# Performance work log

Hardware: AMD Instinct MI355X
Metric: run time of the kernel (lower is better)

Reference implementation:

```python
import jax, jax.numpy as jnp
import numpy as np

N = 50000          # nodes
E = 800000         # edges (before self-loops)
IN_CH = 128
H1, C1 = 8, 32     # layer-1 heads / channels-per-head (concat -> 256)
H2, C2 = 1, 64     # layer-2 (out_channels=64, heads=1)
NEG_SLOPE = 0.2    # PyG GATConv default LeakyReLU slope for attention


def setup_inputs() -> dict:
    key = jax.random.key(0)
    ks = jax.random.split(key, 10)
    x = jax.random.normal(ks[0], (N, IN_CH), dtype=jnp.float32)
    edge_index = jax.random.randint(ks[1], (2, E), 0, N, dtype=jnp.int64)
    s = 0.05
    W1 = jax.random.normal(ks[2], (IN_CH, H1 * C1), dtype=jnp.float32) * s
    a_src1 = jax.random.normal(ks[3], (H1, C1), dtype=jnp.float32) * s
    a_dst1 = jax.random.normal(ks[4], (H1, C1), dtype=jnp.float32) * s
    b1 = jnp.zeros((H1 * C1,), dtype=jnp.float32)
    W2 = jax.random.normal(ks[5], (H1 * C1, H2 * C2), dtype=jnp.float32) * s
    a_src2 = jax.random.normal(ks[6], (H2, C2), dtype=jnp.float32) * s
    a_dst2 = jax.random.normal(ks[7], (H2, C2), dtype=jnp.float32) * s
    b2 = jnp.zeros((H2 * C2,), dtype=jnp.float32)
    return {"x": x, "edge_index": edge_index,
            "W1": W1, "a_src1": a_src1, "a_dst1": a_dst1, "b1": b1,
            "W2": W2, "a_src2": a_src2, "a_dst2": a_dst2, "b2": b2}


def gat_conv(x, src, dst, W, a_src, a_dst, b, heads, ch):
    """PyG GATConv (eval mode): gather -> LeakyReLU attn -> scatter-softmax -> scatter-add."""
    n = x.shape[0]
    h = (x @ W).reshape(n, heads, ch)                     # [N, H, C]
    alpha_s = jnp.einsum('nhc,hc->nh', h, a_src)          # [N, H]
    alpha_d = jnp.einsum('nhc,hc->nh', h, a_dst)
    e = jax.nn.leaky_relu(alpha_s[src] + alpha_d[dst], NEG_SLOPE)  # [E, H]
    # numerically-stable softmax over edges grouped by destination node
    emax = jax.ops.segment_max(e, dst, num_segments=n)
    e = jnp.exp(e - emax[dst])
    denom = jax.ops.segment_sum(e, dst, num_segments=n)
    alpha = e / denom[dst]                                # [E, H]
    out = jax.ops.segment_sum(h[src] * alpha[:, :, None], dst, num_segments=n)  # [N, H, C]
    return out.reshape(n, heads * ch) + b


def reference(x, edge_index, W1, a_src1, a_dst1, b1, W2, a_src2, a_dst2, b2):
    # PyG GATConv adds self-loops by default
    loops = jnp.arange(N, dtype=edge_index.dtype)
    src = jnp.concatenate([edge_index[0], loops])
    dst = jnp.concatenate([edge_index[1], loops])
    h = jax.nn.relu(gat_conv(x, src, dst, W1, a_src1, a_dst1, b1, H1, C1))
    out = jax.nn.relu(gat_conv(h, src, dst, W2, a_src2, a_dst2, b2, H2, C2))
    return out
```

## Files before the change

kernel.cpp:

```cpp
#include <hip/hip_runtime.h>
#include <math.h>

#define NEG_SLOPE 0.2f
__device__ __forceinline__ float leaky(float x) { return fmaxf(x, NEG_SLOPE * x); }

typedef _Float16 f16;
typedef _Float16 f16x2 __attribute__((ext_vector_type(2)));
typedef _Float16 f16x4 __attribute__((ext_vector_type(4)));
typedef _Float16 f16x8 __attribute__((ext_vector_type(8)));
typedef float f32x4 __attribute__((ext_vector_type(4)));

__device__ __forceinline__ int kmap(int lh, int e) {
  return (e < 4) ? lh * 4 + e : 16 + lh * 4 + (e - 4);
}

__global__ void k_count(const int* __restrict__ dst, int* __restrict__ deg, int E) {
  int e = blockIdx.x * blockDim.x + threadIdx.x;
  if (e < E) atomicAdd(&deg[dst[e]], 1);
}

#define W1_TOT (17 * 4 * 64 * 8)
#define W2_TOT (5 * 8 * 64 * 8)
__global__ __launch_bounds__(256) void k_partial_packw(const int* __restrict__ deg,
    int* __restrict__ part, int n, int nb,
    const float* __restrict__ W1, const float* __restrict__ as1f,
    const float* __restrict__ ad1f, const float* __restrict__ W2,
    const float* __restrict__ as2f, const float* __restrict__ ad2f,
    f16* __restrict__ Wp1, f16* __restrict__ Wp2) {
  if ((int)blockIdx.x < nb) {
    __shared__ int s[256];
    int i = blockIdx.x * 256 + threadIdx.x;
    s[threadIdx.x] = (i < n) ? deg[i] : 0;
    __syncthreads();
    for (int off = 128; off > 0; off >>= 1) {
      if (threadIdx.x < off) s[threadIdx.x] += s[threadIdx.x + off];
      __syncthreads();
    }
    if (threadIdx.x == 0) part[blockIdx.x] = s[0];
  }
  int tid = blockIdx.x * 256 + threadIdx.x;
  if (tid < W1_TOT) {
    int e = tid & 7, l = (tid >> 3) & 63, ks = (tid >> 9) & 3, nt = tid >> 11;
    int lh = l >> 4, li = l & 15;
    int k = ks * 32 + kmap(lh, e);
    float v;
    if (nt < 16) {
      v = W1[k * 256 + nt * 16 + li];
    } else {
      int h = li & 7;
      const float* a = (li < 8) ? (as1f + h * 32) : (ad1f + h * 32);
      v = 0.f;
      for (int j = 0; j < 32; ++j) v += W1[k * 256 + h * 32 + j] * a[j];
    }
    Wp1[tid] = (f16)v;
  } else if (tid < W1_TOT + W2_TOT) {
    int t2 = tid - W1_TOT;
    int e = t2 & 7, l = (t2 >> 3) & 63, ks = (t2 >> 9) & 7, nt = t2 >> 12;
    int lh = l >> 4, li = l & 15;
    int k = ks * 32 + kmap(lh, e);
    float v = 0.f;
    if (nt < 4) {
      v = W2[k * 64 + nt * 16 + li];
    } else if (li == 0) {
      for (int j = 0; j < 64; ++j) v += W2[k * 64 + j] * as2f[j];
    } else if (li == 1) {
      for (int j = 0; j < 64; ++j) v += W2[k * 64 + j] * ad2f[j];
    }
    Wp2[t2] = (f16)v;
  }
}

__global__ __launch_bounds__(256) void k_offs(int* __restrict__ deg,
                                              const int* __restrict__ part,
                                              int* __restrict__ offs, int n, int nb) {
  __shared__ int ps[256];
  __shared__ int s[256];
  int t = threadIdx.x;
  ps[t] = (t < nb) ? part[t] : 0;
  __syncthreads();
  for (int off = 1; off < 256; off <<= 1) {
    int u = (t >= off) ? ps[t - off] : 0;
    __syncthreads();
    ps[t] += u;
    __syncthreads();
  }
  int base = (blockIdx.x > 0) ? ps[blockIdx.x - 1] : 0;

  int i = blockIdx.x * 256 + t;
  int v = (i < n) ? deg[i] : 0;
  s[t] = v;
  __syncthreads();
  for (int off = 1; off < 256; off <<= 1) {
    int u = (t >= off) ? s[t - off] : 0;
    __syncthreads();
    s[t] += u;
    __syncthreads();
  }
  int excl = base + s[t] - v;
  if (i < n) {
    offs[i] = excl;
    deg[i] = 0;
  }
  if (i == n - 1) offs[n] = excl + v;
}

__global__ __launch_bounds__(256) void k_fill_gemm1(
    const int* __restrict__ src, const int* __restrict__ dst,
    const int* __restrict__ offs, int* __restrict__ cursor,
    int* __restrict__ col, int E, int fillBlocks,
    const float* __restrict__ x, const f16* __restrict__ Wp1,
    f16* __restrict__ h16, float* __restrict__ as, float* __restrict__ ad,
    int n, int nSlots) {
  if ((int)blockIdx.x < fillBlocks) {
    int e = blockIdx.x * 256 + threadIdx.x;
    if (e >= E) return;
    int d = dst[e];
    int pos = atomicAdd(&cursor[d], 1);
    col[offs[d] + pos] = src[e];
    return;
  }
  int slot = (blockIdx.x - fillBlocks) * 4 + (threadIdx.x >> 6);
  if (slot >= nSlots) return;
  int half = slot & 1;
  int wid = slot >> 1;
  int lane = threadIdx.x & 63, lh = lane >> 4, li = lane & 15;
  size_t arow = (size_t)min(wid * 16 + li, n - 1);
  f16x8 a[4];
#pragma unroll
  for (int ks = 0; ks < 4; ++ks) {
    float4 lo = *(const float4*)&x[arow * 128 + ks * 32 + lh * 4];
    float4 hi = *(const float4*)&x[arow * 128 + ks * 32 + 16 + lh * 4];
    a[ks][0] = (f16)lo.x; a[ks][1] = (f16)lo.y; a[ks][2] = (f16)lo.z; a[ks][3] = (f16)lo.w;
    a[ks][4] = (f16)hi.x; a[ks][5] = (f16)hi.y; a[ks][6] = (f16)hi.z; a[ks][7] = (f16)hi.w;
  }
  int rbase = wid * 16 + lh * 4;
  int ntBeg = half ? 8 : 0;
  int ntEnd = half ? 17 : 8;
  for (int nt = ntBeg; nt < ntEnd; ++nt) {
    f32x4 acc = {0.f, 0.f, 0.f, 0.f};
#pragma unroll
    for (int ks = 0; ks < 4; ++ks) {
      f16x8 b = *(const f16x8*)&Wp1[((nt * 4 + ks) * 64 + lane) * 8];
      acc = __builtin_amdgcn_mfma_f32_16x16x32_f16(a[ks], b, acc, 0, 0, 0);
    }
    if (nt < 16) {
#pragma unroll
      for (int r = 0; r < 4; ++r) {
        int rr = rbase + r;
        if (rr < n) h16[(size_t)rr * 256 + nt * 16 + li] = (f16)acc[r];
      }
    } else {
#pragma unroll
      for (int r = 0; r < 4; ++r) {
        int rr = rbase + r;
        if (rr < n) {
          if (li < 8) as[(size_t)rr * 8 + li] = acc[r];
          else        ad[(size_t)rr * 8 + (li - 8)] = acc[r];
        }
      }
    }
  }
}

__global__ __launch_bounds__(256) void k_gemm2(const f16* __restrict__ R16,
    const f16* __restrict__ Wp2, f16* __restrict__ h2,
    float* __restrict__ as, float* __restrict__ ad, int n, int nWaves) {
  int wid = blockIdx.x * 4 + (threadIdx.x >> 6);
  if (wid >= nWaves) return;
  int lane = threadIdx.x & 63, lh = lane >> 4, li = lane & 15;
  size_t arow = (size_t)min(wid * 16 + li, n - 1);
  f16x8 a[8];
#pragma unroll
  for (int ks = 0; ks < 8; ++ks) {
    f16x4 lo = *(const f16x4*)&R16[arow * 256 + ks * 32 + lh * 4];
    f16x4 hi = *(const f16x4*)&R16[arow * 256 + ks * 32 + 16 + lh * 4];
    a[ks][0] = lo[0]; a[ks][1] = lo[1]; a[ks][2] = lo[2]; a[ks][3] = lo[3];
    a[ks][4] = hi[0]; a[ks][5] = hi[1]; a[ks][6] = hi[2]; a[ks][7] = hi[3];
  }
  int rbase = wid * 16 + lh * 4;
#pragma unroll
  for (int nt = 0; nt < 5; ++nt) {
    f32x4 acc = {0.f, 0.f, 0.f, 0.f};
#pragma unroll
    for (int ks = 0; ks < 8; ++ks) {
      f16x8 b = *(const f16x8*)&Wp2[((nt * 8 + ks) * 64 + lane) * 8];
      acc = __builtin_amdgcn_mfma_f32_16x16x32_f16(a[ks], b, acc, 0, 0, 0);
    }
    if (nt < 4) {
#pragma unroll
      for (int r = 0; r < 4; ++r) {
        int rr = rbase + r;
        if (rr < n) h2[(size_t)rr * 64 + nt * 16 + li] = (f16)acc[r];
      }
    } else {
#pragma unroll
      for (int r = 0; r < 4; ++r) {
        int rr = rbase + r;
        if (rr < n) {
          if (li == 0) as[rr] = acc[r];
          else if (li == 1) ad[rr] = acc[r];
        }
      }
    }
  }
}

__global__ __launch_bounds__(256) void k_agg1(const f16* __restrict__ h16,
    const float* __restrict__ as, const float* __restrict__ ad,
    const int* __restrict__ offs, const int* __restrict__ col,
    const float* __restrict__ b, f16* __restrict__ out, int n) {
  int node = blockIdx.x * 4 + (threadIdx.x >> 6);
  if (node >= n) return;
  node = __builtin_amdgcn_readfirstlane(node);
  int lane = threadIdx.x & 63;
  int head = lane >> 3;
  int c0 = lane * 4;
  int beg = offs[node], end = offs[node + 1];
  float adn = ad[node * 8 + head];

  float denom, ax, ay, az, aw;
  {
    float w = __expf(leaky(as[node * 8 + head] + adn));
    f16x4 g = *(const f16x4*)&h16[(size_t)node * 256 + c0];
    denom = w;
    ax = w * (float)g[0]; ay = w * (float)g[1];
    az = w * (float)g[2]; aw = w * (float)g[3];
  }
  int p = beg;
  for (; p + 8 <= end; p += 8) {
    int s[8];
#pragma unroll
    for (int j = 0; j < 8; ++j) s[j] = col[p + j];
    float e[8];
#pragma unroll
    for (int j = 0; j < 8; ++j) e[j] = as[s[j] * 8 + head];
    f16x4 g[8];
#pragma unroll
    for (int j = 0; j < 8; ++j) g[j] = *(const f16x4*)&h16[(size_t)s[j] * 256 + c0];
    float w[8];
#pragma unroll
    for (int j = 0; j < 8; ++j) w[j] = __expf(leaky(e[j] + adn));
#pragma unroll
    for (int j = 0; j < 8; ++j) {
      denom += w[j];
      ax += w[j] * (float)g[j][0]; ay += w[j] * (float)g[j][1];
      az += w[j] * (float)g[j][2]; aw += w[j] * (float)g[j][3];
    }
  }
  for (; p < end; ++p) {
    int s = col[p];
    float w = __expf(leaky(as[s * 8 + head] + adn));
    f16x4 g = *(const f16x4*)&h16[(size_t)s * 256 + c0];
    denom += w;
    ax += w * (float)g[0]; ay += w * (float)g[1];
    az += w * (float)g[2]; aw += w * (float)g[3];
  }
  float inv = 1.f / denom;
  float4 bv = *(const float4*)&b[c0];
  f16x4 o;
  o[0] = (f16)fmaxf(fmaf(ax, inv, bv.x), 0.f);
  o[1] = (f16)fmaxf(fmaf(ay, inv, bv.y), 0.f);
  o[2] = (f16)fmaxf(fmaf(az, inv, bv.z), 0.f);
  o[3] = (f16)fmaxf(fmaf(aw, inv, bv.w), 0.f);
  __builtin_nontemporal_store(o, (f16x4*)&out[(size_t)node * 256 + c0]);
}

__global__ __launch_bounds__(256) void k_agg2(const f16* __restrict__ h2,
    const float* __restrict__ as, const float* __restrict__ ad,
    const int* __restrict__ offs, const int* __restrict__ col,
    const float* __restrict__ b, float* __restrict__ out, int n) {
  int node = blockIdx.x * 4 + (threadIdx.x >> 6);
  if (node >= n) return;
  node = __builtin_amdgcn_readfirstlane(node);
  int lane = threadIdx.x & 63;
  int es = lane >> 4;
  int c = lane & 15;
  int beg = offs[node], end = offs[node + 1];
  int deg = end - beg;
  float adn = ad[node];

  float a0 = 0.f, a1 = 0.f, a2 = 0.f, a3 = 0.f, wsum = 0.f;
  if (es == 0) {
    float w = __expf(leaky(as[node] + adn));
    f16x4 g = *(const f16x4*)&h2[(size_t)node * 64 + c * 4];
    wsum = w;
    a0 = w * (float)g[0]; a1 = w * (float)g[1];
    a2 = w * (float)g[2]; a3 = w * (float)g[3];
  }
  for (int base = 0; base < deg; base += 16) {
    int s[4]; float e[4]; f16x4 g[4]; float w[4];
#pragma unroll
    for (int q = 0; q < 4; ++q) {
      int idx = base + q * 4 + es;
      s[q] = (idx < deg) ? col[beg + idx] : node;
    }
#pragma unroll
    for (int q = 0; q < 4; ++q) e[q] = as[s[q]];
#pragma unroll
    for (int q = 0; q < 4; ++q) g[q] = *(const f16x4*)&h2[(size_t)s[q] * 64 + c * 4];
#pragma unroll
    for (int q = 0; q < 4; ++q) {
      int idx = base + q * 4 + es;
      w[q] = (idx < deg) ? __expf(leaky(e[q] + adn)) : 0.f;
    }
#pragma unroll
    for (int q = 0; q < 4; ++q) {
      wsum += w[q];
      a0 += w[q] * (float)g[q][0]; a1 += w[q] * (float)g[q][1];
      a2 += w[q] * (float)g[q][2]; a3 += w[q] * (float)g[q][3];
    }
  }
  a0 += __shfl_xor(a0, 16, 64); a1 += __shfl_xor(a1, 16, 64);
  a2 += __shfl_xor(a2, 16, 64); a3 += __shfl_xor(a3, 16, 64);
  wsum += __shfl_xor(wsum, 16, 64);
  a0 += __shfl_xor(a0, 32, 64); a1 += __shfl_xor(a1, 32, 64);
  a2 += __shfl_xor(a2, 32, 64); a3 += __shfl_xor(a3, 32, 64);
  wsum += __shfl_xor(wsum, 32, 64);
  if (es == 0) {
    float inv = 1.f / wsum;
    float4 bv = *(const float4*)&b[c * 4];
    f32x4 o;
    o[0] = fmaxf(fmaf(a0, inv, bv.x), 0.f);
    o[1] = fmaxf(fmaf(a1, inv, bv.y), 0.f);
    o[2] = fmaxf(fmaf(a2, inv, bv.z), 0.f);
    o[3] = fmaxf(fmaf(a3, inv, bv.w), 0.f);
    __builtin_nontemporal_store(o, (f32x4*)&out[(size_t)node * 64 + c * 4]);
  }
}

extern "C" void kernel_launch(void* const* d_in, const int* in_sizes, int n_in,
                              void* d_out, int out_size, void* d_ws, size_t ws_size,
                              hipStream_t stream) {
  const float* x      = (const float*)d_in[0];
  const int*   ei     = (const int*)d_in[1];
  const float* W1     = (const float*)d_in[2];
  const float* a_src1 = (const float*)d_in[3];
  const float* a_dst1 = (const float*)d_in[4];
  const float* b1     = (const float*)d_in[5];
  const float* W2     = (const float*)d_in[6];
  const float* a_src2 = (const float*)d_in[7];
  const float* a_dst2 = (const float*)d_in[8];
  const float* b2     = (const float*)d_in[9];

  int N = in_sizes[0] / 128;
  int E = in_sizes[1] / 2;
  const int* srcI = ei;
  const int* dstI = ei + E;
  int nb = (N + 255) / 256;
  int packBlocks = (W1_TOT + W2_TOT + 255) / 256;
  int ppBlocks = nb > packBlocks ? nb : packBlocks;
  int nWaves = (N + 15) / 16;
  int nSlots1 = nWaves * 2;
  int fillBlocks = (E + 255) / 256;
  int gemm1Blocks = (nSlots1 + 3) / 4;
  int nodeBlocks = (N + 3) / 4;

  char* ws = (char*)d_ws;
  size_t o = 0;
  auto alloc = [&](size_t bytes) -> void* {
    void* p = ws + o;
    o += (bytes + 255) & ~(size_t)255;
    return p;
  };
  f16*   h1f    = (f16*)alloc((size_t)N * 256 * 2);
  f16*   r16    = (f16*)alloc((size_t)N * 256 * 2);
  f16*   h2f    = (f16*)alloc((size_t)N * 64 * 2);
  f16*   Wp1    = (f16*)alloc((size_t)W1_TOT * 2);
  f16*   Wp2    = (f16*)alloc((size_t)W2_TOT * 2);
  float* as1    = (float*)alloc((size_t)N * 8 * 4);
  float* ad1    = (float*)alloc((size_t)N * 8 * 4);
  float* as2    = (float*)alloc((size_t)N * 4);
  float* ad2    = (float*)alloc((size_t)N * 4);
  int*   offs   = (int*)alloc((size_t)(N + 1) * 4);
  int*   cursor = (int*)alloc((size_t)N * 4);
  int*   col    = (int*)alloc((size_t)E * 4);
  int*   part   = (int*)alloc((size_t)nb * 4);

  hipMemsetAsync(cursor, 0, (size_t)N * 4, stream);
  k_count<<<(E + 255) / 256, 256, 0, stream>>>(dstI, cursor, E);
  k_partial_packw<<<ppBlocks, 256, 0, stream>>>(cursor, part, N, nb,
      W1, a_src1, a_dst1, W2, a_src2, a_dst2, Wp1, Wp2);
  k_offs<<<nb, 256, 0, stream>>>(cursor, part, offs, N, nb);

  k_fill_gemm1<<<fillBlocks + gemm1Blocks, 256, 0, stream>>>(
      srcI, dstI, offs, cursor, col, E, fillBlocks,
      x, Wp1, h1f, as1, ad1, N, nSlots1);

  k_agg1<<<nodeBlocks, 256, 0, stream>>>(h1f, as1, ad1, offs, col, b1, r16, N);

  k_gemm2<<<(nWaves + 3) / 4, 256, 0, stream>>>(r16, Wp2, h2f, as2, ad2, N, nWaves);
  k_agg2<<<nodeBlocks, 256, 0, stream>>>(h2f, as2, ad2, offs, col, b2, (float*)d_out, N);
}
```

Before: 216.0 us.

## Fuse layer-1 aggregation with layer-2 GEMM through shared memory

Merges the layer-1 edge aggregation kernel and the layer-2 MFMA GEMM into one kernel. Each block aggregates 16 nodes into an LDS tile, then its four waves split the five output tiles of the 256x(64+2) GEMM. This removes the N x 256 fp16 intermediate write and re-read plus one kernel launch. In exchange, each wave now processes four nodes serially, and the GEMM phase is unbalanced: one wave computes two tiles while the others compute one, with a block barrier between the phases.

```diff
diff --git a/kernel.cpp b/kernel.cpp
--- a/kernel.cpp
+++ b/kernel.cpp
@@ -5,7 +5,6 @@
 __device__ __forceinline__ float leaky(float x) { return fmaxf(x, NEG_SLOPE * x); }
 
 typedef _Float16 f16;
-typedef _Float16 f16x2 __attribute__((ext_vector_type(2)));
 typedef _Float16 f16x4 __attribute__((ext_vector_type(4)));
 typedef _Float16 f16x8 __attribute__((ext_vector_type(8)));
 typedef float f32x4 __attribute__((ext_vector_type(4)));
@@ -162,29 +161,94 @@
   }
 }
 
-__global__ __launch_bounds__(256) void k_gemm2(const f16* __restrict__ R16,
-    const f16* __restrict__ Wp2, f16* __restrict__ h2,
-    float* __restrict__ as, float* __restrict__ ad, int n, int nWaves) {
-  int wid = blockIdx.x * 4 + (threadIdx.x >> 6);
-  if (wid >= nWaves) return;
-  int lane = threadIdx.x & 63, lh = lane >> 4, li = lane & 15;
-  size_t arow = (size_t)min(wid * 16 + li, n - 1);
+#define RPAD 264
+__global__ __launch_bounds__(256) void k_agg1_gemm2(const f16* __restrict__ h16,
+    const float* __restrict__ as, const float* __restrict__ ad,
+    const int* __restrict__ offs, const int* __restrict__ col,
+    const float* __restrict__ b, const f16* __restrict__ Wp2,
+    f16* __restrict__ h2, float* __restrict__ as2, float* __restrict__ ad2, int n) {
+  __shared__ f16 rs[16][RPAD];
+  int wave = threadIdx.x >> 6;
+  int lane = threadIdx.x & 63;
+  int head = lane >> 3;
+  int c0 = lane * 4;
+
+  for (int i = 0; i < 4; ++i) {
+    int rl = wave * 4 + i;
+    int node = blockIdx.x * 16 + rl;
+    if (node >= n) {
+      f16x4 z = {(f16)0.f, (f16)0.f, (f16)0.f, (f16)0.f};
+      *(f16x4*)&rs[rl][c0] = z;
+      continue;
+    }
+    node = __builtin_amdgcn_readfirstlane(node);
+    int beg = offs[node], end = offs[node + 1];
+    float adn = ad[node * 8 + head];
+
+    float denom, ax, ay, az, aw;
+    {
+      float w = __expf(leaky(as[node * 8 + head] + adn));
+      f16x4 g = *(const f16x4*)&h16[(size_t)node * 256 + c0];
+      denom = w;
+      ax = w * (float)g[0]; ay = w * (float)g[1];
+      az = w * (float)g[2]; aw = w * (float)g[3];
+    }
+    int p = beg;
+    for (; p + 8 <= end; p += 8) {
+      int s[8];
+#pragma unroll
+      for (int j = 0; j < 8; ++j) s[j] = col[p + j];
+      float e[8];
+#pragma unroll
+      for (int j = 0; j < 8; ++j) e[j] = as[s[j] * 8 + head];
+      f16x4 g[8];
+#pragma unroll
+      for (int j = 0; j < 8; ++j) g[j] = *(const f16x4*)&h16[(size_t)s[j] * 256 + c0];
+      float w[8];
+#pragma unroll
+      for (int j = 0; j < 8; ++j) w[j] = __expf(leaky(e[j] + adn));
+#pragma unroll
+      for (int j = 0; j < 8; ++j) {
+        denom += w[j];
+        ax += w[j] * (float)g[j][0]; ay += w[j] * (float)g[j][1];
+        az += w[j] * (float)g[j][2]; aw += w[j] * (float)g[j][3];
+      }
+    }
+    for (; p < end; ++p) {
+      int s = col[p];
+      float w = __expf(leaky(as[s * 8 + head] + adn));
+      f16x4 g = *(const f16x4*)&h16[(size_t)s * 256 + c0];
+      denom += w;
+      ax += w * (float)g[0]; ay += w * (float)g[1];
+      az += w * (float)g[2]; aw += w * (float)g[3];
+    }
+    float inv = 1.f / denom;
+    float4 bv = *(const float4*)&b[c0];
+    f16x4 o;
+    o[0] = (f16)fmaxf(fmaf(ax, inv, bv.x), 0.f);
+    o[1] = (f16)fmaxf(fmaf(ay, inv, bv.y), 0.f);
+    o[2] = (f16)fmaxf(fmaf(az, inv, bv.z), 0.f);
+    o[3] = (f16)fmaxf(fmaf(aw, inv, bv.w), 0.f);
+    *(f16x4*)&rs[rl][c0] = o;
+  }
+  __syncthreads();
+
+  int lh = lane >> 4, li = lane & 15;
   f16x8 a[8];
 #pragma unroll
   for (int ks = 0; ks < 8; ++ks) {
-    f16x4 lo = *(const f16x4*)&R16[arow * 256 + ks * 32 + lh * 4];
-    f16x4 hi = *(const f16x4*)&R16[arow * 256 + ks * 32 + 16 + lh * 4];
+    f16x4 lo = *(const f16x4*)&rs[li][ks * 32 + lh * 4];
+    f16x4 hi = *(const f16x4*)&rs[li][ks * 32 + 16 + lh * 4];
     a[ks][0] = lo[0]; a[ks][1] = lo[1]; a[ks][2] = lo[2]; a[ks][3] = lo[3];
     a[ks][4] = hi[0]; a[ks][5] = hi[1]; a[ks][6] = hi[2]; a[ks][7] = hi[3];
   }
-  int rbase = wid * 16 + lh * 4;
-#pragma unroll
-  for (int nt = 0; nt < 5; ++nt) {
+  int rbase = blockIdx.x * 16 + lh * 4;
+  for (int nt = wave; nt < 5; nt += 4) {
     f32x4 acc = {0.f, 0.f, 0.f, 0.f};
 #pragma unroll
     for (int ks = 0; ks < 8; ++ks) {
-      f16x8 b = *(const f16x8*)&Wp2[((nt * 8 + ks) * 64 + lane) * 8];
-      acc = __builtin_amdgcn_mfma_f32_16x16x32_f16(a[ks], b, acc, 0, 0, 0);
+      f16x8 bb = *(const f16x8*)&Wp2[((nt * 8 + ks) * 64 + lane) * 8];
+      acc = __builtin_amdgcn_mfma_f32_16x16x32_f16(a[ks], bb, acc, 0, 0, 0);
     }
     if (nt < 4) {
 #pragma unroll
@@ -197,72 +261,12 @@
       for (int r = 0; r < 4; ++r) {
         int rr = rbase + r;
         if (rr < n) {
-          if (li == 0) as[rr] = acc[r];
-          else if (li == 1) ad[rr] = acc[r];
+          if (li == 0) as2[rr] = acc[r];
+          else if (li == 1) ad2[rr] = acc[r];
         }
       }
     }
   }
-}
-
-__global__ __launch_bounds__(256) void k_agg1(const f16* __restrict__ h16,
-    const float* __restrict__ as, const float* __restrict__ ad,
-    const int* __restrict__ offs, const int* __restrict__ col,
-    const float* __restrict__ b, f16* __restrict__ out, int n) {
-  int node = blockIdx.x * 4 + (threadIdx.x >> 6);
-  if (node >= n) return;
-  node = __builtin_amdgcn_readfirstlane(node);
-  int lane = threadIdx.x & 63;
-  int head = lane >> 3;
-  int c0 = lane * 4;
-  int beg = offs[node], end = offs[node + 1];
-  float adn = ad[node * 8 + head];
-
-  float denom, ax, ay, az, aw;
-  {
-    float w = __expf(leaky(as[node * 8 + head] + adn));
-    f16x4 g = *(const f16x4*)&h16[(size_t)node * 256 + c0];
-    denom = w;
-    ax = w * (float)g[0]; ay = w * (float)g[1];
-    az = w * (float)g[2]; aw = w * (float)g[3];
-  }
-  int p = beg;
-  for (; p + 8 <= end; p += 8) {
-    int s[8];
-#pragma unroll
-    for (int j = 0; j < 8; ++j) s[j] = col[p + j];
-    float e[8];
-#pragma unroll
-    for (int j = 0; j < 8; ++j) e[j] = as[s[j] * 8 + head];
-    f16x4 g[8];
-#pragma unroll
-    for (int j = 0; j < 8; ++j) g[j] = *(const f16x4*)&h16[(size_t)s[j] * 256 + c0];
-    float w[8];
-#pragma unroll
-    for (int j = 0; j < 8; ++j) w[j] = __expf(leaky(e[j] + adn));
-#pragma unroll
-    for (int j = 0; j < 8; ++j) {
-      denom += w[j];
-      ax += w[j] * (float)g[j][0]; ay += w[j] * (float)g[j][1];
-      az += w[j] * (float)g[j][2]; aw += w[j] * (float)g[j][3];
-    }
-  }
-  for (; p < end; ++p) {
-    int s = col[p];
-    float w = __expf(leaky(as[s * 8 + head] + adn));
-    f16x4 g = *(const f16x4*)&h16[(size_t)s * 256 + c0];
-    denom += w;
-    ax += w * (float)g[0]; ay += w * (float)g[1];
-    az += w * (float)g[2]; aw += w * (float)g[3];
-  }
-  float inv = 1.f / denom;
-  float4 bv = *(const float4*)&b[c0];
-  f16x4 o;
-  o[0] = (f16)fmaxf(fmaf(ax, inv, bv.x), 0.f);
-  o[1] = (f16)fmaxf(fmaf(ay, inv, bv.y), 0.f);
-  o[2] = (f16)fmaxf(fmaf(az, inv, bv.z), 0.f);
-  o[3] = (f16)fmaxf(fmaf(aw, inv, bv.w), 0.f);
-  __builtin_nontemporal_store(o, (f16x4*)&out[(size_t)node * 256 + c0]);
 }
 
 __global__ __launch_bounds__(256) void k_agg2(const f16* __restrict__ h2,
@@ -354,6 +358,7 @@
   int fillBlocks = (E + 255) / 256;
   int gemm1Blocks = (nSlots1 + 3) / 4;
   int nodeBlocks = (N + 3) / 4;
+  int aggBlocks = (N + 15) / 16;
 
   char* ws = (char*)d_ws;
   size_t o = 0;
@@ -363,7 +368,6 @@
     return p;
   };
   f16*   h1f    = (f16*)alloc((size_t)N * 256 * 2);
-  f16*   r16    = (f16*)alloc((size_t)N * 256 * 2);
   f16*   h2f    = (f16*)alloc((size_t)N * 64 * 2);
   f16*   Wp1    = (f16*)alloc((size_t)W1_TOT * 2);
   f16*   Wp2    = (f16*)alloc((size_t)W2_TOT * 2);
@@ -386,8 +390,8 @@
       srcI, dstI, offs, cursor, col, E, fillBlocks,
       x, Wp1, h1f, as1, ad1, N, nSlots1);
 
-  k_agg1<<<nodeBlocks, 256, 0, stream>>>(h1f, as1, ad1, offs, col, b1, r16, N);
-
-  k_gemm2<<<(nWaves + 3) / 4, 256, 0, stream>>>(r16, Wp2, h2f, as2, ad2, N, nWaves);
+  k_agg1_gemm2<<<aggBlocks, 256, 0, stream>>>(h1f, as1, ad1, offs, col, b1,
+                                              Wp2, h2f, as2, ad2, N);
+
   k_agg2<<<nodeBlocks, 256, 0, stream>>>(h2f, as2, ad2, offs, col, b2, (float*)d_out, N);
 }
```

After: 210.8 us. 2.4% less time.
